# Optimization experiments

Measured on AMD Instinct MI355X. Metric: run time of the kernel, lower is better.

## Reference

```python
import jax, jax.numpy as jnp
import numpy as np

N_NODES = 100000
N_EDGES = 1600000
IN_CH = 128
HEADS = 4
OUT_CH = 32
NEG_SLOPE = 0.2
EPS = 1e-10


def setup_inputs() -> dict:
    key = jax.random.key(0)
    k1, k2, k3, k4 = jax.random.split(key, 4)
    x = jax.random.normal(k1, (N_NODES, IN_CH), dtype=jnp.float32)
    edge_index = jax.random.randint(k2, (2, N_EDGES), 0, N_NODES, dtype=jnp.int64)
    # small scale keeps exp(-leakyrelu(score)) numerically tame
    W = jax.random.normal(k3, (IN_CH, HEADS * OUT_CH), dtype=jnp.float32) * 0.05
    attention = jax.random.normal(k4, (HEADS, 2 * OUT_CH), dtype=jnp.float32) * 0.05
    bias = jnp.zeros((HEADS * OUT_CH,), dtype=jnp.float32)
    return {"x": x, "edge_index": edge_index, "W": W, "attention": attention, "bias": bias}


def reference(x, edge_index, W, attention, bias):
    N = x.shape[0]
    H, two_o = attention.shape
    O = two_o // 2
    # shared fc_src == fc_tgt (in_channels is an int in the original)
    h = (x @ W).reshape(N, H, O)  # [N, H, O]
    # attention vector splits over the concat [h_src || h_tgt]
    a_src, a_tgt = attention[:, :O], attention[:, O:]
    s_src = jnp.einsum('nho,ho->nh', h, a_src)  # [N, H]
    s_tgt = jnp.einsum('nho,ho->nh', h, a_tgt)  # [N, H]
    src, tgt = edge_index[0], edge_index[1]
    score = s_src[src] + s_tgt[tgt]  # [E, H]
    # NOTE: original applies exp to the NEGATED LeakyReLU output
    e = jnp.exp(-jax.nn.leaky_relu(score, NEG_SLOPE))  # [E, H]
    # numerator: sum_j e_ij * h_src[j] scattered to target nodes
    num = jax.ops.segment_sum(e[:, :, None] * h[src], tgt, num_segments=N)  # [N, H, O]
    den = jax.ops.segment_sum(e, tgt, num_segments=N)  # [N, H]
    out = num / jnp.clip(den, EPS, None)[:, :, None]
    out = out.reshape(N, H * O)  # concat=True
    return out + bias
```

## Files before the change

kernel.cpp:

```cpp
#include <hip/hip_runtime.h>
#include <stdint.h>


#define NN 100000
#define EE 1600000
#define INCH 128
#define HO 128
#define HEADS 4
#define OUTC 32

#define BSH 8
#define NBUCK ((NN + 255) >> BSH)
#define CAPBK 5120
#define CHA 4096
#define ABLK ((EE + CHA - 1) / CHA)

typedef unsigned short ushort_t;
typedef unsigned int uint_t;
typedef __attribute__((ext_vector_type(8))) short bf16x8;
typedef __attribute__((ext_vector_type(4))) float f32x4;

__device__ __forceinline__ float bfl(uint_t u) { return __uint_as_float(u << 16); }
__device__ __forceinline__ float bfh(uint_t u) { return __uint_as_float(u & 0xffff0000u); }
__device__ __forceinline__ uint_t f2bf(float f) {
    uint_t u = __float_as_uint(f);
    u = (u + 0x7fffu + ((u >> 16) & 1u)) >> 16;
    return u;
}
__device__ __forceinline__ float att_w(float sc) {
    return __expf(-(sc > 0.f ? sc : 0.2f * sc));
}

__global__ __launch_bounds__(256) void prepW_k(const float* __restrict__ W,
                                               ushort_t* __restrict__ gWtHi,
                                               ushort_t* __restrict__ gWtLo) {
    const int gidx = blockIdx.x * 256 + threadIdx.x;
    const int col = gidx & 127;
    const int k = gidx >> 7;
    const float v = W[k * 128 + col];
    const uint_t h = f2bf(v);
    const uint_t lo = f2bf(v - bfl(h));
    gWtHi[col * 128 + k] = (ushort_t)h;
    gWtLo[col * 128 + k] = (ushort_t)lo;
}

__global__ __launch_bounds__(256) void gemm_h(const float* __restrict__ x,
                                              const ushort_t* __restrict__ gWtHi,
                                              const ushort_t* __restrict__ gWtLo,
                                              const float* __restrict__ att,
                                              ushort_t* __restrict__ hb,
                                              float* __restrict__ s_src,
                                              float* __restrict__ s_tgt) {
    __shared__ __align__(16) char smem[16384];
    ushort_t* xHi  = (ushort_t*)smem;
    ushort_t* xLo  = (ushort_t*)(smem + 8192);
    const int tid = threadIdx.x;
    const int row0 = blockIdx.x * 32;

    const int lane = tid & 63;
    const int w = tid >> 6;
    const int l15 = lane & 15;
    const int g = lane >> 4;
    const int swz = (l15 & 7) << 4;

    bf16x8 bh[2][4], bl[2][4];
    {
        const ushort_t* pH = gWtHi + (size_t)(w * 32 + l15) * 128 + g * 8;
        const ushort_t* pL = gWtLo + (size_t)(w * 32 + l15) * 128 + g * 8;
#pragma unroll
        for (int ntl = 0; ntl < 2; ++ntl)
#pragma unroll
            for (int ks = 0; ks < 4; ++ks) {
                bh[ntl][ks] = *(const bf16x8*)(pH + ntl * 16 * 128 + ks * 32);
                bl[ntl][ks] = *(const bf16x8*)(pL + ntl * 16 * 128 + ks * 32);
            }
    }

    {
        const float4* x4 = (const float4*)(x + (size_t)row0 * INCH);
#pragma unroll
        for (int j = 0; j < 4; ++j) {
            const int i = tid + 256 * j;
            const int row = i >> 5;
            const int k4 = i & 31;
            const float4 v = x4[i];
            const uint_t h0 = f2bf(v.x), h1 = f2bf(v.y), h2 = f2bf(v.z), h3 = f2bf(v.w);
            const uint_t l0 = f2bf(v.x - bfl(h0));
            const uint_t l1 = f2bf(v.y - bfl(h1));
            const uint_t l2 = f2bf(v.z - bfl(h2));
            const uint_t l3 = f2bf(v.w - bfl(h3));
            const int byteOff = (row * 256 + k4 * 8) ^ ((row & 7) << 4);
            *(uint2*)((char*)xHi + byteOff) = make_uint2(h0 | (h1 << 16), h2 | (h3 << 16));
            *(uint2*)((char*)xLo + byteOff) = make_uint2(l0 | (l1 << 16), l2 | (l3 << 16));
        }
    }
    __syncthreads();

    f32x4 acc[2][2] = {};
#pragma unroll
    for (int ks = 0; ks < 4; ++ks) {
        const int kb = ks * 64 + g * 16;
        const bf16x8 a0h = *(const bf16x8*)((char*)xHi + ((l15 * 256 + kb) ^ swz));
        const bf16x8 a1h = *(const bf16x8*)((char*)xHi + (((16 + l15) * 256 + kb) ^ swz));
        const bf16x8 a0l = *(const bf16x8*)((char*)xLo + ((l15 * 256 + kb) ^ swz));
        const bf16x8 a1l = *(const bf16x8*)((char*)xLo + (((16 + l15) * 256 + kb) ^ swz));
        acc[0][0] = __builtin_amdgcn_mfma_f32_16x16x32_bf16(a0h, bh[0][ks], acc[0][0], 0, 0, 0);
        acc[0][1] = __builtin_amdgcn_mfma_f32_16x16x32_bf16(a0h, bh[1][ks], acc[0][1], 0, 0, 0);
        acc[1][0] = __builtin_amdgcn_mfma_f32_16x16x32_bf16(a1h, bh[0][ks], acc[1][0], 0, 0, 0);
        acc[1][1] = __builtin_amdgcn_mfma_f32_16x16x32_bf16(a1h, bh[1][ks], acc[1][1], 0, 0, 0);
        acc[0][0] = __builtin_amdgcn_mfma_f32_16x16x32_bf16(a0h, bl[0][ks], acc[0][0], 0, 0, 0);
        acc[0][1] = __builtin_amdgcn_mfma_f32_16x16x32_bf16(a0h, bl[1][ks], acc[0][1], 0, 0, 0);
        acc[1][0] = __builtin_amdgcn_mfma_f32_16x16x32_bf16(a1h, bl[0][ks], acc[1][0], 0, 0, 0);
        acc[1][1] = __builtin_amdgcn_mfma_f32_16x16x32_bf16(a1h, bl[1][ks], acc[1][1], 0, 0, 0);
        acc[0][0] = __builtin_amdgcn_mfma_f32_16x16x32_bf16(a0l, bh[0][ks], acc[0][0], 0, 0, 0);
        acc[0][1] = __builtin_amdgcn_mfma_f32_16x16x32_bf16(a0l, bh[1][ks], acc[0][1], 0, 0, 0);
        acc[1][0] = __builtin_amdgcn_mfma_f32_16x16x32_bf16(a1l, bh[0][ks], acc[1][0], 0, 0, 0);
        acc[1][1] = __builtin_amdgcn_mfma_f32_16x16x32_bf16(a1l, bh[1][ks], acc[1][1], 0, 0, 0);
    }

#pragma unroll
    for (int mt = 0; mt < 2; ++mt)
#pragma unroll
        for (int ntl = 0; ntl < 2; ++ntl) {
            const int col = w * 32 + ntl * 16 + l15;
#pragma unroll
            for (int r = 0; r < 4; ++r) {
                const int row = row0 + mt * 16 + g * 4 + r;
                hb[(size_t)row * HO + col] = (ushort_t)f2bf(acc[mt][ntl][r]);
            }
        }

    const float cs0 = att[w * 64 + l15];
    const float cs1 = att[w * 64 + 16 + l15];
    const float ct0 = att[w * 64 + 32 + l15];
    const float ct1 = att[w * 64 + 48 + l15];
#pragma unroll
    for (int mt = 0; mt < 2; ++mt)
#pragma unroll
        for (int r = 0; r < 4; ++r) {
            float ps = acc[mt][0][r] * cs0 + acc[mt][1][r] * cs1;
            float pt = acc[mt][0][r] * ct0 + acc[mt][1][r] * ct1;
#pragma unroll
            for (int d = 1; d < 16; d <<= 1) {
                ps += __shfl_xor(ps, d, 64);
                pt += __shfl_xor(pt, d, 64);
            }
            if (l15 == 0) {
                const int row = row0 + mt * 16 + g * 4 + r;
                s_src[row * 4 + w] = ps;
                s_tgt[row * 4 + w] = pt;
            }
        }
}

__global__ __launch_bounds__(512) void bucketA_k(const int* __restrict__ ei,
                                                 int* __restrict__ gcur,
                                                 uint_t* __restrict__ grec) {
    __shared__ int hist[NBUCK];
    __shared__ int gbase[NBUCK];
    __shared__ int lcur[NBUCK];
    const int tid = threadIdx.x;
    const int e0 = blockIdx.x * CHA;
    const int cnt = min(CHA, EE - e0);

    for (int b = tid; b < NBUCK; b += 512) hist[b] = 0;
    __syncthreads();
    for (int i = tid; i < cnt; i += 512)
        atomicAdd(&hist[ei[EE + e0 + i] >> BSH], 1);
    __syncthreads();
    for (int b = tid; b < NBUCK; b += 512) {
        const int h = hist[b];
        gbase[b] = b * CAPBK + (h ? atomicAdd(&gcur[b], h) : 0);
        lcur[b] = 0;
    }
    __syncthreads();
    for (int i = tid; i < cnt; i += 512) {
        const int src = ei[e0 + i];
        const int tgt = ei[EE + e0 + i];
        const int b = tgt >> BSH;
        const int p = atomicAdd(&lcur[b], 1);
        grec[gbase[b] + p] = (uint_t)src | ((uint_t)(tgt & 255) << 17);
    }
}

__global__ __launch_bounds__(1024) void bucketB_k(const int* __restrict__ bucketCnt,
                                                  const uint_t* __restrict__ grec,
                                                  const float* __restrict__ s_src,
                                                  const float* __restrict__ s_tgt,
                                                  int2* __restrict__ offs2,
                                                  int* __restrict__ sorted_src,
                                                  float4* __restrict__ wgt) {
    __shared__ int cur[256];
    __shared__ int scn[256];
    __shared__ uint_t sbuf[CAPBK];
    const int tid = threadIdx.x;
    const int b = blockIdx.x;
    const int n0 = b << BSH;
    const int nn = min(256, NN - n0);
    const int R0 = b * CAPBK;
    const int cnt = min(bucketCnt[b], CAPBK);

    if (tid < 256) cur[tid] = 0;
    __syncthreads();
    uint_t r0v = 0xFFFFFFFFu, r1v = 0xFFFFFFFFu, r2v = 0xFFFFFFFFu,
           r3v = 0xFFFFFFFFu, r4v = 0xFFFFFFFFu;
    {
        int i = tid;
        if (i < cnt) { r0v = grec[R0 + i]; atomicAdd(&cur[r0v >> 17], 1); } i += 1024;
        if (i < cnt) { r1v = grec[R0 + i]; atomicAdd(&cur[r1v >> 17], 1); } i += 1024;
        if (i < cnt) { r2v = grec[R0 + i]; atomicAdd(&cur[r2v >> 17], 1); } i += 1024;
        if (i < cnt) { r3v = grec[R0 + i]; atomicAdd(&cur[r3v >> 17], 1); } i += 1024;
        if (i < cnt) { r4v = grec[R0 + i]; atomicAdd(&cur[r4v >> 17], 1); }
    }
    __syncthreads();
    int v = 0;
    if (tid < 256) { v = cur[tid]; scn[tid] = v; }
    __syncthreads();
#pragma unroll
    for (int off = 1; off < 256; off <<= 1) {
        int u = (tid < 256 && tid >= off) ? scn[tid - off] : 0;
        __syncthreads();
        if (tid < 256) scn[tid] += u;
        __syncthreads();
    }
    if (tid < 256) {
        const int ex = scn[tid] - v;
        cur[tid] = ex;
        if (tid < nn) offs2[n0 + tid] = make_int2(R0 + ex, R0 + ex + v);
    }
    __syncthreads();
    if (r0v != 0xFFFFFFFFu) sbuf[atomicAdd(&cur[r0v >> 17], 1)] = r0v;
    if (r1v != 0xFFFFFFFFu) sbuf[atomicAdd(&cur[r1v >> 17], 1)] = r1v;
    if (r2v != 0xFFFFFFFFu) sbuf[atomicAdd(&cur[r2v >> 17], 1)] = r2v;
    if (r3v != 0xFFFFFFFFu) sbuf[atomicAdd(&cur[r3v >> 17], 1)] = r3v;
    if (r4v != 0xFFFFFFFFu) sbuf[atomicAdd(&cur[r4v >> 17], 1)] = r4v;
    __syncthreads();
    for (int i = tid; i < cnt; i += 1024) {
        const uint_t r = sbuf[i];
        const int src = (int)(r & 0x1FFFF);
        const int tl = (int)(r >> 17);
        sorted_src[R0 + i] = src;
        const float4 ss = *(const float4*)(s_src + src * 4);
        const float4 st = *(const float4*)(s_tgt + (n0 + tl) * 4);
        float4 wv;
        wv.x = att_w(ss.x + st.x);
        wv.y = att_w(ss.y + st.y);
        wv.z = att_w(ss.z + st.z);
        wv.w = att_w(ss.w + st.w);
        wgt[R0 + i] = wv;
    }
}

template <bool PRED>
__device__ __forceinline__ void gat8(const float* __restrict__ wgt,
                                     const ushort_t* __restrict__ hb,
                                     int srcv, int p0, int p1, int base, int e, int m,
                                     int hd, int c0, float& ax, float& ay, float& wsum) {
    int s[8]; float w[8]; uint_t v[8];
#pragma unroll
    for (int j = 0; j < 8; ++j)
        s[j] = __builtin_amdgcn_readlane(srcv, (e + j) & 63);
#pragma unroll
    for (int j = 0; j < 8; ++j) {
        int idx = p0 + base + e + j;
        if (PRED) idx = min(idx, p1 - 1);
        const float wl = wgt[(uint_t)idx * 4u + hd];
        w[j] = (PRED && (e + j >= m)) ? 0.f : wl;
    }
#pragma unroll
    for (int j = 0; j < 8; ++j)
        v[j] = *(const uint_t*)(hb + (uint_t)(s[j] * HO + c0));
#pragma unroll
    for (int j = 0; j < 8; ++j) {
        ax = fmaf(w[j], bfl(v[j]), ax);
        ay = fmaf(w[j], bfh(v[j]), ay);
    }
    wsum += ((w[0] + w[1]) + (w[2] + w[3])) + ((w[4] + w[5]) + (w[6] + w[7]));
}

__global__ __launch_bounds__(256) void gather_k(const int2* __restrict__ offs2,
                                                const int* __restrict__ sorted_src,
                                                const float* __restrict__ wgt,
                                                const ushort_t* __restrict__ hb,
                                                const float* __restrict__ bias,
                                                float* __restrict__ out) {
    const int n = blockIdx.x * 4 + (threadIdx.x >> 6);
    const int l = threadIdx.x & 63;
    const int c0 = l * 2;
    const int hd = l >> 4;
    const int2 pr = offs2[n];
    const int p0 = pr.x, p1 = pr.y;
    const int deg = p1 - p0;
    float ax = 0.f, ay = 0.f, wsum = 0.f;
    for (int base = 0; base < deg; base += 64) {
        const int m = min(deg - base, 64);
        const int srcv = sorted_src[p0 + base + ((l < m) ? l : 0)];
        int e = 0;
        for (; e + 8 <= m; e += 8)
            gat8<false>(wgt, hb, srcv, p0, p1, base, e, m, hd, c0, ax, ay, wsum);
        if (e < m)
            gat8<true>(wgt, hb, srcv, p0, p1, base, e, m, hd, c0, ax, ay, wsum);
    }
    const float inv = 1.f / fmaxf(wsum, 1e-10f);
    float2 o;
    o.x = ax * inv + bias[c0];
    o.y = ay * inv + bias[c0 + 1];
    *(float2*)(out + (size_t)n * HO + c0) = o;
}

extern "C" void kernel_launch(void* const* d_in, const int* in_sizes, int n_in,
                              void* d_out, int out_size, void* d_ws, size_t ws_size,
                              hipStream_t stream) {
    const float* x    = (const float*)d_in[0];
    const int*   ei   = (const int*)d_in[1];
    const float* W    = (const float*)d_in[2];
    const float* att  = (const float*)d_in[3];
    const float* bias = (const float*)d_in[4];
    float* out = (float*)d_out;

    char* ws = (char*)d_ws;
    const size_t HB_B  = (size_t)NN * HO * 2;
    const size_t SS_B  = (size_t)NBUCK * CAPBK * 4;
    const size_t GR_B  = (size_t)NBUCK * CAPBK * 4;
    const size_t WG_B  = (size_t)NBUCK * CAPBK * 16;
    const size_t S_B   = (size_t)NN * HEADS * 4;
    const size_t OF_B  = ((size_t)NN * 8 + 15) & ~15ull;
    const size_t GC_B  = ((size_t)NBUCK * 4 + 15) & ~15ull;
    const size_t WT_B  = 32768;

    size_t o = 0;
    ushort_t* hb         = (ushort_t*)(ws + o); o += HB_B;
    int*      sorted_src = (int*)(ws + o); o += SS_B;
    uint_t*   grec       = (uint_t*)(ws + o); o += GR_B;
    float4*   wgt        = (float4*)(ws + o); o += WG_B;
    float*    ssrc       = (float*)(ws + o); o += S_B;
    float*    stgt       = (float*)(ws + o); o += S_B;
    int2*     offs2      = (int2*)(ws + o); o += OF_B;
    int*      gcur       = (int*)(ws + o); o += GC_B;
    ushort_t* gWtHi      = (ushort_t*)(ws + o); o += WT_B;
    ushort_t* gWtLo      = (ushort_t*)(ws + o); o += WT_B;

    (void)hipMemsetAsync(gcur, 0, GC_B, stream);

    prepW_k<<<64, 256, 0, stream>>>(W, gWtHi, gWtLo);
    gemm_h<<<NN / 32, 256, 0, stream>>>(x, gWtHi, gWtLo, att,
                                        hb, ssrc, stgt);
    bucketA_k<<<ABLK, 512, 0, stream>>>(ei, gcur, grec);
    bucketB_k<<<NBUCK, 1024, 0, stream>>>(gcur, grec, ssrc, stgt,
                                          offs2, sorted_src, wgt);
    gather_k<<<NN / 4, 256, 0, stream>>>(offs2, sorted_src, (const float*)wgt,
                                         hb, bias, out);
}
```

Before: 243.6 us.

## Fuse GEMM and edge bucketing into one launch, fold memset into prepW

Merges the projection GEMM kernel and the first edge-bucketing pass into a single launch, with the extra blocks doing the bucketing so the two independent phases can run concurrently on the GPU. The bucket counter reset moves from a separate memset into the weight-prep kernel. This removes two launches and the idle gap between GEMM and bucketing. In exchange the bucketing blocks now use 256 threads instead of 512 and share the GEMM's 16 KB LDS footprint, and heterogeneous blocks in one grid may balance less evenly.

Measured after the change: 244.1 us. No clear change (+0.2%).

```diff
diff --git a/kernel.cpp b/kernel.cpp
--- a/kernel.cpp
+++ b/kernel.cpp
@@ -14,6 +14,7 @@
 #define CAPBK 5120
 #define CHA 4096
 #define ABLK ((EE + CHA - 1) / CHA)
+#define GEMMB (NN / 32)
 
 typedef unsigned short ushort_t;
 typedef unsigned int uint_t;
@@ -33,7 +34,11 @@
 
 __global__ __launch_bounds__(256) void prepW_k(const float* __restrict__ W,
                                                ushort_t* __restrict__ gWtHi,
-                                               ushort_t* __restrict__ gWtLo) {
+                                               ushort_t* __restrict__ gWtLo,
+                                               int* __restrict__ gcur) {
+    if (blockIdx.x == 0) {
+        for (int i = threadIdx.x; i < NBUCK; i += 256) gcur[i] = 0;
+    }
     const int gidx = blockIdx.x * 256 + threadIdx.x;
     const int col = gidx & 127;
     const int k = gidx >> 7;
@@ -44,17 +49,49 @@
     gWtLo[col * 128 + k] = (ushort_t)lo;
 }
 
-__global__ __launch_bounds__(256) void gemm_h(const float* __restrict__ x,
-                                              const ushort_t* __restrict__ gWtHi,
-                                              const ushort_t* __restrict__ gWtLo,
-                                              const float* __restrict__ att,
-                                              ushort_t* __restrict__ hb,
-                                              float* __restrict__ s_src,
-                                              float* __restrict__ s_tgt) {
+__global__ __launch_bounds__(256) void fusedGA_k(const float* __restrict__ x,
+                                                 const ushort_t* __restrict__ gWtHi,
+                                                 const ushort_t* __restrict__ gWtLo,
+                                                 const float* __restrict__ att,
+                                                 ushort_t* __restrict__ hb,
+                                                 float* __restrict__ s_src,
+                                                 float* __restrict__ s_tgt,
+                                                 const int* __restrict__ ei,
+                                                 int* __restrict__ gcur,
+                                                 uint_t* __restrict__ grec) {
     __shared__ __align__(16) char smem[16384];
-    ushort_t* xHi  = (ushort_t*)smem;
-    ushort_t* xLo  = (ushort_t*)(smem + 8192);
     const int tid = threadIdx.x;
+
+    if (blockIdx.x >= GEMMB) {
+        int* hist  = (int*)smem;
+        int* gbase = hist + NBUCK;
+        int* lcur  = gbase + NBUCK;
+        const int e0 = (blockIdx.x - GEMMB) * CHA;
+        const int cnt = min(CHA, EE - e0);
+
+        for (int b = tid; b < NBUCK; b += 256) hist[b] = 0;
+        __syncthreads();
+        for (int i = tid; i < cnt; i += 256)
+            atomicAdd(&hist[ei[EE + e0 + i] >> BSH], 1);
+        __syncthreads();
+        for (int b = tid; b < NBUCK; b += 256) {
+            const int h = hist[b];
+            gbase[b] = b * CAPBK + (h ? atomicAdd(&gcur[b], h) : 0);
+            lcur[b] = 0;
+        }
+        __syncthreads();
+        for (int i = tid; i < cnt; i += 256) {
+            const int src = ei[e0 + i];
+            const int tgt = ei[EE + e0 + i];
+            const int b = tgt >> BSH;
+            const int p = atomicAdd(&lcur[b], 1);
+            grec[gbase[b] + p] = (uint_t)src | ((uint_t)(tgt & 255) << 17);
+        }
+        return;
+    }
+
+    ushort_t* xHi = (ushort_t*)smem;
+    ushort_t* xLo = (ushort_t*)(smem + 8192);
     const int row0 = blockIdx.x * 32;
 
     const int lane = tid & 63;
@@ -151,36 +188,6 @@
                 s_tgt[row * 4 + w] = pt;
             }
         }
-}
-
-__global__ __launch_bounds__(512) void bucketA_k(const int* __restrict__ ei,
-                                                 int* __restrict__ gcur,
-                                                 uint_t* __restrict__ grec) {
-    __shared__ int hist[NBUCK];
-    __shared__ int gbase[NBUCK];
-    __shared__ int lcur[NBUCK];
-    const int tid = threadIdx.x;
-    const int e0 = blockIdx.x * CHA;
-    const int cnt = min(CHA, EE - e0);
-
-    for (int b = tid; b < NBUCK; b += 512) hist[b] = 0;
-    __syncthreads();
-    for (int i = tid; i < cnt; i += 512)
-        atomicAdd(&hist[ei[EE + e0 + i] >> BSH], 1);
-    __syncthreads();
-    for (int b = tid; b < NBUCK; b += 512) {
-        const int h = hist[b];
-        gbase[b] = b * CAPBK + (h ? atomicAdd(&gcur[b], h) : 0);
-        lcur[b] = 0;
-    }
-    __syncthreads();
-    for (int i = tid; i < cnt; i += 512) {
-        const int src = ei[e0 + i];
-        const int tgt = ei[EE + e0 + i];
-        const int b = tgt >> BSH;
-        const int p = atomicAdd(&lcur[b], 1);
-        grec[gbase[b] + p] = (uint_t)src | ((uint_t)(tgt & 255) << 17);
-    }
 }
 
 __global__ __launch_bounds__(1024) void bucketB_k(const int* __restrict__ bucketCnt,
@@ -340,12 +347,10 @@
     ushort_t* gWtHi      = (ushort_t*)(ws + o); o += WT_B;
     ushort_t* gWtLo      = (ushort_t*)(ws + o); o += WT_B;
 
-    (void)hipMemsetAsync(gcur, 0, GC_B, stream);
-
-    prepW_k<<<64, 256, 0, stream>>>(W, gWtHi, gWtLo);
-    gemm_h<<<NN / 32, 256, 0, stream>>>(x, gWtHi, gWtLo, att,
-                                        hb, ssrc, stgt);
-    bucketA_k<<<ABLK, 512, 0, stream>>>(ei, gcur, grec);
+    prepW_k<<<64, 256, 0, stream>>>(W, gWtHi, gWtLo, gcur);
+    fusedGA_k<<<GEMMB + ABLK, 256, 0, stream>>>(x, gWtHi, gWtLo, att,
+                                                hb, ssrc, stgt,
+                                                ei, gcur, grec);
     bucketB_k<<<NBUCK, 1024, 0, stream>>>(gcur, grec, ssrc, stgt,
                                           offs2, sorted_src, wgt);
     gather_k<<<NN / 4, 256, 0, stream>>>(offs2, sorted_src, (const float*)wgt,
```

## Merge independent GEMM and bucketing stages into shared launches for overlap

Applied to the files above, without the earlier changes.

Fuses the W-prep kernel with the edge-bucketing pass, and the per-bucket local sort with the projection GEMM, into two heterogeneous kernels so independent work runs concurrently. The attention-weight computation moves into its own flat kernel over all slots. The gather reads the packed sorted record and masks out the source index, which removes the separate sorted_src array. This adds an extra launch and a pass over the padded slot space, and the local sort now uses 256 threads instead of 1024.

Result: no change. 241.9 us (-0.7%).

```diff
diff --git a/kernel.cpp b/kernel.cpp
--- a/kernel.cpp
+++ b/kernel.cpp
@@ -14,6 +14,8 @@
 #define CAPBK 5120
 #define CHA 4096
 #define ABLK ((EE + CHA - 1) / CHA)
+#define GEMMB (NN / 32)
+#define NSLOT (NBUCK * CAPBK)
 
 typedef unsigned short ushort_t;
 typedef unsigned int uint_t;
@@ -31,31 +33,108 @@
     return __expf(-(sc > 0.f ? sc : 0.2f * sc));
 }
 
-__global__ __launch_bounds__(256) void prepW_k(const float* __restrict__ W,
-                                               ushort_t* __restrict__ gWtHi,
-                                               ushort_t* __restrict__ gWtLo) {
-    const int gidx = blockIdx.x * 256 + threadIdx.x;
-    const int col = gidx & 127;
-    const int k = gidx >> 7;
-    const float v = W[k * 128 + col];
-    const uint_t h = f2bf(v);
-    const uint_t lo = f2bf(v - bfl(h));
-    gWtHi[col * 128 + k] = (ushort_t)h;
-    gWtLo[col * 128 + k] = (ushort_t)lo;
-}
-
-__global__ __launch_bounds__(256) void gemm_h(const float* __restrict__ x,
-                                              const ushort_t* __restrict__ gWtHi,
-                                              const ushort_t* __restrict__ gWtLo,
-                                              const float* __restrict__ att,
-                                              ushort_t* __restrict__ hb,
-                                              float* __restrict__ s_src,
-                                              float* __restrict__ s_tgt) {
-    __shared__ __align__(16) char smem[16384];
-    ushort_t* xHi  = (ushort_t*)smem;
-    ushort_t* xLo  = (ushort_t*)(smem + 8192);
+__global__ __launch_bounds__(512) void fusedPA_k(const int* __restrict__ ei,
+                                                 int* __restrict__ gcur,
+                                                 uint_t* __restrict__ grec,
+                                                 const float* __restrict__ W,
+                                                 ushort_t* __restrict__ gWtHi,
+                                                 ushort_t* __restrict__ gWtLo) {
+    __shared__ int hist[NBUCK];
+    __shared__ int gbase[NBUCK];
+    __shared__ int lcur[NBUCK];
     const int tid = threadIdx.x;
-    const int row0 = blockIdx.x * 32;
+
+    if (blockIdx.x >= ABLK) {
+        const int gidx = (blockIdx.x - ABLK) * 512 + tid;
+        const int col = gidx & 127;
+        const int k = gidx >> 7;
+        const float v = W[k * 128 + col];
+        const uint_t h = f2bf(v);
+        const uint_t lo = f2bf(v - bfl(h));
+        gWtHi[col * 128 + k] = (ushort_t)h;
+        gWtLo[col * 128 + k] = (ushort_t)lo;
+        return;
+    }
+    const int e0 = blockIdx.x * CHA;
+    const int cnt = min(CHA, EE - e0);
+
+    for (int b = tid; b < NBUCK; b += 512) hist[b] = 0;
+    __syncthreads();
+    for (int i = tid; i < cnt; i += 512)
+        atomicAdd(&hist[ei[EE + e0 + i] >> BSH], 1);
+    __syncthreads();
+    for (int b = tid; b < NBUCK; b += 512) {
+        const int h = hist[b];
+        gbase[b] = b * CAPBK + (h ? atomicAdd(&gcur[b], h) : 0);
+        lcur[b] = 0;
+    }
+    __syncthreads();
+    for (int i = tid; i < cnt; i += 512) {
+        const int src = ei[e0 + i];
+        const int tgt = ei[EE + e0 + i];
+        const int b = tgt >> BSH;
+        const int p = atomicAdd(&lcur[b], 1);
+        grec[gbase[b] + p] = (uint_t)src | ((uint_t)(tgt & 255) << 17);
+    }
+}
+
+__global__ __launch_bounds__(256) void fusedGS_k(const uint_t* __restrict__ grec,
+                                                 const int* __restrict__ gcur,
+                                                 int2* __restrict__ offs2,
+                                                 uint_t* __restrict__ srec,
+                                                 const float* __restrict__ x,
+                                                 const ushort_t* __restrict__ gWtHi,
+                                                 const ushort_t* __restrict__ gWtLo,
+                                                 const float* __restrict__ att,
+                                                 ushort_t* __restrict__ hb,
+                                                 float* __restrict__ s_src,
+                                                 float* __restrict__ s_tgt) {
+    __shared__ __align__(16) char smem[22528];
+    const int tid = threadIdx.x;
+
+    if (blockIdx.x < NBUCK) {
+        uint_t* sbuf = (uint_t*)smem;
+        int* cur = (int*)(smem + 20480);
+        int* scn = (int*)(smem + 21504);
+        const int b = blockIdx.x;
+        const int n0 = b << BSH;
+        const int nn = min(256, NN - n0);
+        const int R0 = b * CAPBK;
+        const int cnt = min(gcur[b], CAPBK);
+
+        cur[tid] = 0;
+        __syncthreads();
+        for (int i = tid; i < cnt; i += 256)
+            atomicAdd(&cur[grec[R0 + i] >> 17], 1);
+        __syncthreads();
+        const int v = cur[tid];
+        scn[tid] = v;
+        __syncthreads();
+#pragma unroll
+        for (int off = 1; off < 256; off <<= 1) {
+            int u = (tid >= off) ? scn[tid - off] : 0;
+            __syncthreads();
+            scn[tid] += u;
+            __syncthreads();
+        }
+        const int ex = scn[tid] - v;
+        cur[tid] = ex;
+        if (tid < nn) offs2[n0 + tid] = make_int2(R0 + ex, R0 + ex + v);
+        __syncthreads();
+        for (int i = tid; i < cnt; i += 256) {
+            const uint_t r = grec[R0 + i];
+            const int p = atomicAdd(&cur[r >> 17], 1);
+            sbuf[p] = r;
+        }
+        __syncthreads();
+        for (int i = tid; i < cnt; i += 256)
+            srec[R0 + i] = sbuf[i];
+        return;
+    }
+
+    ushort_t* xHi = (ushort_t*)smem;
+    ushort_t* xLo = (ushort_t*)(smem + 8192);
+    const int row0 = (blockIdx.x - NBUCK) * 32;
 
     const int lane = tid & 63;
     const int w = tid >> 6;
@@ -153,113 +232,43 @@
         }
 }
 
-__global__ __launch_bounds__(512) void bucketA_k(const int* __restrict__ ei,
-                                                 int* __restrict__ gcur,
-                                                 uint_t* __restrict__ grec) {
-    __shared__ int hist[NBUCK];
-    __shared__ int gbase[NBUCK];
-    __shared__ int lcur[NBUCK];
-    const int tid = threadIdx.x;
-    const int e0 = blockIdx.x * CHA;
-    const int cnt = min(CHA, EE - e0);
-
-    for (int b = tid; b < NBUCK; b += 512) hist[b] = 0;
-    __syncthreads();
-    for (int i = tid; i < cnt; i += 512)
-        atomicAdd(&hist[ei[EE + e0 + i] >> BSH], 1);
-    __syncthreads();
-    for (int b = tid; b < NBUCK; b += 512) {
-        const int h = hist[b];
-        gbase[b] = b * CAPBK + (h ? atomicAdd(&gcur[b], h) : 0);
-        lcur[b] = 0;
-    }
-    __syncthreads();
-    for (int i = tid; i < cnt; i += 512) {
-        const int src = ei[e0 + i];
-        const int tgt = ei[EE + e0 + i];
-        const int b = tgt >> BSH;
-        const int p = atomicAdd(&lcur[b], 1);
-        grec[gbase[b] + p] = (uint_t)src | ((uint_t)(tgt & 255) << 17);
-    }
-}
-
-__global__ __launch_bounds__(1024) void bucketB_k(const int* __restrict__ bucketCnt,
-                                                  const uint_t* __restrict__ grec,
-                                                  const float* __restrict__ s_src,
-                                                  const float* __restrict__ s_tgt,
-                                                  int2* __restrict__ offs2,
-                                                  int* __restrict__ sorted_src,
-                                                  float4* __restrict__ wgt) {
-    __shared__ int cur[256];
-    __shared__ int scn[256];
-    __shared__ uint_t sbuf[CAPBK];
-    const int tid = threadIdx.x;
-    const int b = blockIdx.x;
-    const int n0 = b << BSH;
-    const int nn = min(256, NN - n0);
-    const int R0 = b * CAPBK;
-    const int cnt = min(bucketCnt[b], CAPBK);
-
-    if (tid < 256) cur[tid] = 0;
-    __syncthreads();
-    uint_t r0v = 0xFFFFFFFFu, r1v = 0xFFFFFFFFu, r2v = 0xFFFFFFFFu,
-           r3v = 0xFFFFFFFFu, r4v = 0xFFFFFFFFu;
-    {
-        int i = tid;
-        if (i < cnt) { r0v = grec[R0 + i]; atomicAdd(&cur[r0v >> 17], 1); } i += 1024;
-        if (i < cnt) { r1v = grec[R0 + i]; atomicAdd(&cur[r1v >> 17], 1); } i += 1024;
-        if (i < cnt) { r2v = grec[R0 + i]; atomicAdd(&cur[r2v >> 17], 1); } i += 1024;
-        if (i < cnt) { r3v = grec[R0 + i]; atomicAdd(&cur[r3v >> 17], 1); } i += 1024;
-        if (i < cnt) { r4v = grec[R0 + i]; atomicAdd(&cur[r4v >> 17], 1); }
-    }
-    __syncthreads();
-    int v = 0;
-    if (tid < 256) { v = cur[tid]; scn[tid] = v; }
-    __syncthreads();
-#pragma unroll
-    for (int off = 1; off < 256; off <<= 1) {
-        int u = (tid < 256 && tid >= off) ? scn[tid - off] : 0;
-        __syncthreads();
-        if (tid < 256) scn[tid] += u;
-        __syncthreads();
-    }
-    if (tid < 256) {
-        const int ex = scn[tid] - v;
-        cur[tid] = ex;
-        if (tid < nn) offs2[n0 + tid] = make_int2(R0 + ex, R0 + ex + v);
-    }
-    __syncthreads();
-    if (r0v != 0xFFFFFFFFu) sbuf[atomicAdd(&cur[r0v >> 17], 1)] = r0v;
-    if (r1v != 0xFFFFFFFFu) sbuf[atomicAdd(&cur[r1v >> 17], 1)] = r1v;
-    if (r2v != 0xFFFFFFFFu) sbuf[atomicAdd(&cur[r2v >> 17], 1)] = r2v;
-    if (r3v != 0xFFFFFFFFu) sbuf[atomicAdd(&cur[r3v >> 17], 1)] = r3v;
-    if (r4v != 0xFFFFFFFFu) sbuf[atomicAdd(&cur[r4v >> 17], 1)] = r4v;
-    __syncthreads();
-    for (int i = tid; i < cnt; i += 1024) {
-        const uint_t r = sbuf[i];
-        const int src = (int)(r & 0x1FFFF);
-        const int tl = (int)(r >> 17);
-        sorted_src[R0 + i] = src;
-        const float4 ss = *(const float4*)(s_src + src * 4);
-        const float4 st = *(const float4*)(s_tgt + (n0 + tl) * 4);
-        float4 wv;
-        wv.x = att_w(ss.x + st.x);
-        wv.y = att_w(ss.y + st.y);
-        wv.z = att_w(ss.z + st.z);
-        wv.w = att_w(ss.w + st.w);
-        wgt[R0 + i] = wv;
+__global__ __launch_bounds__(256) void wgt_k(const uint_t* __restrict__ srec,
+                                             const int* __restrict__ gcur,
+                                             const float* __restrict__ s_src,
+                                             const float* __restrict__ s_tgt,
+                                             float4* __restrict__ wgt) {
+    const int base = blockIdx.x * 2048 + threadIdx.x;
+#pragma unroll
+    for (int j = 0; j < 8; ++j) {
+        const int slot = base + j * 256;
+        if (slot >= NSLOT) return;
+        const int b = (uint_t)slot / CAPBK;
+        const int i = slot - b * CAPBK;
+        if (i < gcur[b]) {
+            const uint_t r = srec[slot];
+            const int src = (int)(r & 0x1FFFF);
+            const int tgt = (b << BSH) + (int)(r >> 17);
+            const float4 ss = *(const float4*)(s_src + src * 4);
+            const float4 st = *(const float4*)(s_tgt + tgt * 4);
+            float4 wv;
+            wv.x = att_w(ss.x + st.x);
+            wv.y = att_w(ss.y + st.y);
+            wv.z = att_w(ss.z + st.z);
+            wv.w = att_w(ss.w + st.w);
+            wgt[slot] = wv;
+        }
     }
 }
 
 template <bool PRED>
 __device__ __forceinline__ void gat8(const float* __restrict__ wgt,
                                      const ushort_t* __restrict__ hb,
-                                     int srcv, int p0, int p1, int base, int e, int m,
+                                     uint_t srcv, int p0, int p1, int base, int e, int m,
                                      int hd, int c0, float& ax, float& ay, float& wsum) {
-    int s[8]; float w[8]; uint_t v[8];
+    uint_t s[8]; float w[8]; uint_t v[8];
 #pragma unroll
     for (int j = 0; j < 8; ++j)
-        s[j] = __builtin_amdgcn_readlane(srcv, (e + j) & 63);
+        s[j] = __builtin_amdgcn_readlane(srcv, (e + j) & 63) & 0x1FFFFu;
 #pragma unroll
     for (int j = 0; j < 8; ++j) {
         int idx = p0 + base + e + j;
@@ -279,7 +288,7 @@
 }
 
 __global__ __launch_bounds__(256) void gather_k(const int2* __restrict__ offs2,
-                                                const int* __restrict__ sorted_src,
+                                                const uint_t* __restrict__ srec,
                                                 const float* __restrict__ wgt,
                                                 const ushort_t* __restrict__ hb,
                                                 const float* __restrict__ bias,
@@ -294,7 +303,7 @@
     float ax = 0.f, ay = 0.f, wsum = 0.f;
     for (int base = 0; base < deg; base += 64) {
         const int m = min(deg - base, 64);
-        const int srcv = sorted_src[p0 + base + ((l < m) ? l : 0)];
+        const uint_t srcv = srec[p0 + base + ((l < m) ? l : 0)];
         int e = 0;
         for (; e + 8 <= m; e += 8)
             gat8<false>(wgt, hb, srcv, p0, p1, base, e, m, hd, c0, ax, ay, wsum);
@@ -320,9 +329,9 @@
 
     char* ws = (char*)d_ws;
     const size_t HB_B  = (size_t)NN * HO * 2;
-    const size_t SS_B  = (size_t)NBUCK * CAPBK * 4;
-    const size_t GR_B  = (size_t)NBUCK * CAPBK * 4;
-    const size_t WG_B  = (size_t)NBUCK * CAPBK * 16;
+    const size_t SR_B  = (size_t)NSLOT * 4;
+    const size_t GR_B  = (size_t)NSLOT * 4;
+    const size_t WG_B  = (size_t)NSLOT * 16;
     const size_t S_B   = (size_t)NN * HEADS * 4;
     const size_t OF_B  = ((size_t)NN * 8 + 15) & ~15ull;
     const size_t GC_B  = ((size_t)NBUCK * 4 + 15) & ~15ull;
@@ -330,7 +339,7 @@
 
     size_t o = 0;
     ushort_t* hb         = (ushort_t*)(ws + o); o += HB_B;
-    int*      sorted_src = (int*)(ws + o); o += SS_B;
+    uint_t*   srec       = (uint_t*)(ws + o); o += SR_B;
     uint_t*   grec       = (uint_t*)(ws + o); o += GR_B;
     float4*   wgt        = (float4*)(ws + o); o += WG_B;
     float*    ssrc       = (float*)(ws + o); o += S_B;
@@ -342,12 +351,13 @@
 
     (void)hipMemsetAsync(gcur, 0, GC_B, stream);
 
-    prepW_k<<<64, 256, 0, stream>>>(W, gWtHi, gWtLo);
-    gemm_h<<<NN / 32, 256, 0, stream>>>(x, gWtHi, gWtLo, att,
-                                        hb, ssrc, stgt);
-    bucketA_k<<<ABLK, 512, 0, stream>>>(ei, gcur, grec);
-    bucketB_k<<<NBUCK, 1024, 0, stream>>>(gcur, grec, ssrc, stgt,
-                                          offs2, sorted_src, wgt);
-    gather_k<<<NN / 4, 256, 0, stream>>>(offs2, sorted_src, (const float*)wgt,
+    fusedPA_k<<<ABLK + 32, 512, 0, stream>>>(ei, gcur, grec,
+                                             W, gWtHi, gWtLo);
+    fusedGS_k<<<NBUCK + GEMMB, 256, 0, stream>>>(grec, gcur, offs2, srec,
+                                                 x, gWtHi, gWtLo, att,
+                                                 hb, ssrc, stgt);
+    wgt_k<<<(NSLOT + 2047) / 2048, 256, 0, stream>>>(srec, gcur,
+                                                     ssrc, stgt, wgt);
+    gather_k<<<NN / 4, 256, 0, stream>>>(offs2, srec, (const float*)wgt,
                                          hb, bias, out);
 }
```
